# Kernel tuning notes

Hardware: AMD Instinct MI355X
Metric: run time of the kernel (lower is better)

Reference implementation:

```python
import jax, jax.numpy as jnp
import numpy as np

LATENT, H, A, L, BOS = 256, 512, 64, 128, 0


def setup_inputs() -> dict:
    key = jax.random.key(0)
    ks = jax.random.split(key, 20)
    s = 0.05
    return {
        "latent": jax.random.normal(ks[0], (4096, LATENT), jnp.float32),
        "target": jax.random.normal(ks[1], (4096, L, A), jnp.float32),
        # latent dense decoder: Linear(LATENT,H), Tanh, Linear(H,H), Tanh, Linear(H,H)
        "Wd1": jax.random.normal(ks[2], (H, LATENT), jnp.float32) * s,
        "bd1": jnp.zeros((H,), jnp.float32),
        "Wd2": jax.random.normal(ks[3], (H, H), jnp.float32) * s,
        "bd2": jnp.zeros((H,), jnp.float32),
        "Wd3": jax.random.normal(ks[4], (H, H), jnp.float32) * s,
        "bd3": jnp.zeros((H,), jnp.float32),
        # GRU (torch layout: W_ih [3H,A], W_hh [3H,H], gate order r,z,n)
        "W_ih": jax.random.normal(ks[5], (3 * H, A), jnp.float32) * s,
        "W_hh": jax.random.normal(ks[6], (3 * H, H), jnp.float32) * s,
        "b_ih": jnp.zeros((3 * H,), jnp.float32),
        "b_hh": jnp.zeros((3 * H,), jnp.float32),
        # per-step dense decoder: Linear(H,H), Tanh, Linear(H,A), Tanh, Linear(A,A)
        "Wm1": jax.random.normal(ks[7], (H, H), jnp.float32) * s,
        "bm1": jnp.zeros((H,), jnp.float32),
        "Wm2": jax.random.normal(ks[8], (A, H), jnp.float32) * s,
        "bm2": jnp.zeros((A,), jnp.float32),
        "Wm3": jax.random.normal(ks[9], (A, A), jnp.float32) * s,
        "bm3": jnp.zeros((A,), jnp.float32),
    }


def reference(latent, target, Wd1, bd1, Wd2, bd2, Wd3, bd3,
              W_ih, W_hh, b_ih, b_hh, Wm1, bm1, Wm2, bm2, Wm3, bm3):
    B = latent.shape[0]
    # initial hidden from latent: Linear-Tanh-Linear-Tanh-Linear
    h = jnp.tanh(latent @ Wd1.T + bd1)
    h = jnp.tanh(h @ Wd2.T + bd2)
    h = h @ Wd3.T + bd3  # [B, H]

    # BOS pseudo one-hot: -16 everywhere, +16 at BOS index
    bos = jnp.full((B, A), -16.0, jnp.float32).at[:, BOS].set(16.0)

    # teacher forcing: step i (1..L-1) consumes [bos, target[:,1], ..., target[:,L-2]]
    xs = jnp.concatenate([bos[None], jnp.swapaxes(target[:, 1:L - 1], 0, 1)], axis=0)  # [L-1, B, A]

    def step(h, x):
        gi = x @ W_ih.T + b_ih  # [B, 3H]
        gh = h @ W_hh.T + b_hh
        ir, iz, inn = jnp.split(gi, 3, axis=-1)
        hr, hz, hn = jnp.split(gh, 3, axis=-1)
        r = jax.nn.sigmoid(ir + hr)
        z = jax.nn.sigmoid(iz + hz)
        n = jnp.tanh(inn + r * hn)
        h_new = (1.0 - z) * n + z * h
        p = jnp.tanh(h_new @ Wm1.T + bm1)
        p = jnp.tanh(p @ Wm2.T + bm2)
        pred = p @ Wm3.T + bm3  # [B, A]
        return h_new, pred

    _, preds = jax.lax.scan(step, h, xs)  # preds: [L-1, B, A]
    y = jnp.concatenate([bos[None], preds], axis=0)  # [L, B, A]
    return jnp.swapaxes(y, 0, 1)  # [B, L, A]
```

## Files before the change

### kernel.cpp

```cpp
#include <hip/hip_runtime.h>
#include <math.h>
#include <stdint.h>

#define BATCH 4096
#define LATENT 256
#define H 512
#define A 64
#define SEQL 128
#define KCAT 576
#define CT 8

typedef __bf16 bf16x8 __attribute__((ext_vector_type(8)));
typedef float f32x4 __attribute__((ext_vector_type(4)));

__device__ __forceinline__ uint16_t f2bf(float f) {
    union { float f; uint32_t u; } v; v.f = f;
    uint32_t u = v.u + 0x7FFFu + ((v.u >> 16) & 1u);
    return (uint16_t)(u >> 16);
}

__device__ __forceinline__ float fast_sig(float x) {
    return __fdividef(1.0f, 1.0f + __expf(-x));
}
__device__ __forceinline__ float fast_tanh(float x) {
    return __fdividef(2.0f, 1.0f + __expf(-2.0f * x)) - 1.0f;
}

__device__ __forceinline__ f32x4 mfma16(bf16x8 a, bf16x8 b, f32x4 c) {
    return __builtin_amdgcn_mfma_f32_16x16x32_bf16(a, b, c, 0, 0, 0);
}

__device__ __forceinline__ void load_lds16(const void* g, void* l) {
    __builtin_amdgcn_global_load_lds(
        (const __attribute__((address_space(1))) uint32_t*)g,
        (__attribute__((address_space(3))) uint32_t*)l, 16, 0, 0);
}


__global__ __launch_bounds__(256) void cvt_bf16_kernel(const float* __restrict__ src,
                                                       uint16_t* __restrict__ dst, int n) {
    int idx = (blockIdx.x * 256 + threadIdx.x) * 4;
    if (idx < n) {
        float4 v = *(const float4*)(src + idx);
        dst[idx + 0] = f2bf(v.x); dst[idx + 1] = f2bf(v.y);
        dst[idx + 2] = f2bf(v.z); dst[idx + 3] = f2bf(v.w);
    }
}

__global__ __launch_bounds__(256) void wcat_kernel(const float* __restrict__ W_ih,
                                                   const float* __restrict__ W_hh,
                                                   uint16_t* __restrict__ Wcat) {
    int idx = blockIdx.x * 256 + threadIdx.x;
    if (idx < 1536 * KCAT) {
        int row = idx / KCAT, col = idx - row * KCAT;
        float v = (col < 64) ? W_ih[row * 64 + col] : W_hh[row * 512 + col - 64];
        Wcat[idx] = f2bf(v);
    }
}

__global__ __launch_bounds__(256) void bias_kernel(const float* __restrict__ b_ih,
                                                   const float* __restrict__ b_hh,
                                                   float* __restrict__ biases) {
    int idx = blockIdx.x * 256 + threadIdx.x;
    if (idx < 2048) {
        int seg = idx >> 9, j = idx & 511;
        float v;
        if (seg == 0) v = b_ih[j] + b_hh[j];
        else if (seg == 1) v = b_ih[512 + j] + b_hh[512 + j];
        else if (seg == 2) v = b_ih[1024 + j];
        else v = b_hh[1024 + j];
        biases[idx] = v;
    }
}

__global__ __launch_bounds__(256) void bos_kernel(uint16_t* __restrict__ bosb,
                                                  float* __restrict__ out) {
    int idx = blockIdx.x * 256 + threadIdx.x;
    int a = idx & (A - 1);
    int b = idx >> 6;
    float v = (a == 0) ? 16.0f : -16.0f;
    bosb[idx] = f2bf(v);
    out[(size_t)b * SEQL * A + a] = v;
}

template <int BN>
__global__ __launch_bounds__(256)
void gemm_kernel(const uint16_t* __restrict__ Abf, int lda,
                 const uint16_t* __restrict__ Wbf,
                 const float* __restrict__ bias,
                 uint16_t* __restrict__ outb, float* __restrict__ outf,
                 int ldc, int K, int flags, int t0)
{
    __shared__ __align__(16) uint16_t As[128 * 32];
    __shared__ __align__(16) uint16_t Bs[BN * 32];

    const int tid = threadIdx.x;
    const int w = tid >> 6, l = tid & 63;
    const int quad = l >> 4, lan = l & 15;
    const int m0 = blockIdx.y * 128;
    const int n0 = blockIdx.x * BN;

    constexpr int MI = (BN == 128) ? 4 : 2;
    const int wm = (BN == 128) ? ((w >> 1) * 64) : (w * 32);
    const int wn = (BN == 128) ? ((w & 1) * 64) : 0;

    f32x4 acc[MI][4];
#pragma unroll
    for (int i = 0; i < MI; ++i)
#pragma unroll
        for (int j = 0; j < 4; ++j) acc[i][j] = (f32x4){0.f, 0.f, 0.f, 0.f};

    const int arow = (l >> 2);
    const int kc8 = (l & 3) * 8;

    for (int k0 = 0; k0 < K; k0 += 32) {
        __syncthreads();
#pragma unroll
        for (int i = 0; i < 2; ++i) {
            int row = i * 64 + w * 16 + arow;
            load_lds16(Abf + (size_t)(m0 + row) * lda + k0 + kc8,
                       As + i * 2048 + w * 512 + l * 8);
        }
#pragma unroll
        for (int i = 0; i < BN / 64; ++i) {
            int row = i * 64 + w * 16 + arow;
            load_lds16(Wbf + (size_t)(n0 + row) * K + k0 + kc8,
                       Bs + i * 2048 + w * 512 + l * 8);
        }
        __syncthreads();

        bf16x8 af[MI], bf[4];
#pragma unroll
        for (int mi = 0; mi < MI; ++mi)
            af[mi] = *(const bf16x8*)(As + (wm + mi * 16 + lan) * 32 + quad * 8);
#pragma unroll
        for (int nj = 0; nj < 4; ++nj)
            bf[nj] = *(const bf16x8*)(Bs + (wn + nj * 16 + lan) * 32 + quad * 8);
#pragma unroll
        for (int mi = 0; mi < MI; ++mi)
#pragma unroll
            for (int nj = 0; nj < 4; ++nj)
                acc[mi][nj] = mfma16(af[mi], bf[nj], acc[mi][nj]);
    }

    const bool do_tanh = flags & 1;
    const bool mapseq = flags & 2;
#pragma unroll
    for (int mi = 0; mi < MI; ++mi) {
#pragma unroll
        for (int nj = 0; nj < 4; ++nj) {
#pragma unroll
            for (int reg = 0; reg < 4; ++reg) {
                int m = m0 + wm + mi * 16 + quad * 4 + reg;
                int n = n0 + wn + nj * 16 + lan;
                float v = acc[mi][nj][reg] + bias[n];
                if (do_tanh) v = fast_tanh(v);
                if (mapseq) {
                    int b = m & (BATCH - 1), tloc = m >> 12;
                    outf[(size_t)b * SEQL * A + (size_t)(t0 + tloc + 1) * A + n] = v;
                } else {
                    if (outf) outf[(size_t)m * ldc + n] = v;
                    if (outb) outb[(size_t)m * ldc + n] = f2bf(v);
                }
            }
        }
    }
}

__global__ __launch_bounds__(128)
void gru_step_kernel(const uint16_t* __restrict__ xsrc, int sx,
                     const uint16_t* __restrict__ hsrc,
                     const uint16_t* __restrict__ Wcat,
                     const float* __restrict__ biases,
                     const float* __restrict__ hprev,
                     float* __restrict__ hout_f,
                     uint16_t* __restrict__ hout_b)
{
    __shared__ __align__(16) uint16_t As[64 * 32];
    __shared__ __align__(16) uint16_t Bs[192 * 32];

    const int tid = threadIdx.x;
    const int w = tid >> 6, l = tid & 63;
    const int quad = l >> 4, lan = l & 15;
    const int m0 = blockIdx.y * 64;
    const int j0 = blockIdx.x * 64;

    f32x4 acc[2][4][4];
#pragma unroll
    for (int a = 0; a < 2; ++a)
#pragma unroll
        for (int b = 0; b < 4; ++b)
#pragma unroll
            for (int c = 0; c < 4; ++c) acc[a][b][c] = (f32x4){0.f, 0.f, 0.f, 0.f};

    const int arow = (l >> 2);
    const int kc8 = (l & 3) * 8;

    for (int it = 0; it < KCAT / 32; ++it) {
        const int k0 = it * 32;
        const bool xseg = (k0 < 64);
        __syncthreads();
        {
            const uint16_t* src = xseg ? xsrc : hsrc;
            const int stride = xseg ? sx : H;
            const int kc = xseg ? k0 : (k0 - 64);
#pragma unroll
            for (int i = 0; i < 2; ++i) {
                int row = i * 32 + w * 16 + arow;
                load_lds16(src + (size_t)(m0 + row) * stride + kc + kc8,
                           As + i * 1024 + w * 512 + l * 8);
            }
        }
#pragma unroll
        for (int i = 0; i < 6; ++i) {
            int row = i * 32 + w * 16 + arow;
            int g = row >> 6, n = row & 63;
            load_lds16(Wcat + (size_t)((g << 9) + j0 + n) * KCAT + k0 + kc8,
                       Bs + i * 1024 + w * 512 + l * 8);
        }
        __syncthreads();

        bf16x8 af[2];
#pragma unroll
        for (int mi = 0; mi < 2; ++mi)
            af[mi] = *(const bf16x8*)(As + (w * 32 + mi * 16 + lan) * 32 + quad * 8);
#pragma unroll
        for (int g = 0; g < 3; ++g) {
            const int tgt = (g == 2) ? (xseg ? 2 : 3) : g;
#pragma unroll
            for (int nj = 0; nj < 4; ++nj) {
                bf16x8 bfr = *(const bf16x8*)(Bs + (g * 64 + nj * 16 + lan) * 32 + quad * 8);
                acc[0][tgt][nj] = mfma16(af[0], bfr, acc[0][tgt][nj]);
                acc[1][tgt][nj] = mfma16(af[1], bfr, acc[1][tgt][nj]);
            }
        }
    }

    const float* br = biases;
    const float* bz = biases + 512;
    const float* bi = biases + 1024;
    const float* bh = biases + 1536;
#pragma unroll
    for (int mi = 0; mi < 2; ++mi) {
#pragma unroll
        for (int nj = 0; nj < 4; ++nj) {
#pragma unroll
            for (int reg = 0; reg < 4; ++reg) {
                int m = m0 + w * 32 + mi * 16 + quad * 4 + reg;
                int j = j0 + nj * 16 + lan;
                float R = acc[mi][0][nj][reg] + br[j];
                float Z = acc[mi][1][nj][reg] + bz[j];
                float I = acc[mi][2][nj][reg] + bi[j];
                float Hh = acc[mi][3][nj][reg] + bh[j];
                float r = fast_sig(R);
                float z = fast_sig(Z);
                float nn = fast_tanh(I + r * Hh);
                float hp = hprev[(size_t)m * H + j];
                float hv = (1.0f - z) * nn + z * hp;
                hout_f[(size_t)m * H + j] = hv;
                hout_b[(size_t)m * H + j] = f2bf(hv);
            }
        }
    }
}


extern "C" void kernel_launch(void* const* d_in, const int* in_sizes, int n_in,
                              void* d_out, int out_size, void* d_ws, size_t ws_size,
                              hipStream_t stream)
{
    const float* latent = (const float*)d_in[0];
    const float* target = (const float*)d_in[1];
    const float* Wd1 = (const float*)d_in[2];
    const float* bd1 = (const float*)d_in[3];
    const float* Wd2 = (const float*)d_in[4];
    const float* bd2 = (const float*)d_in[5];
    const float* Wd3 = (const float*)d_in[6];
    const float* bd3 = (const float*)d_in[7];
    const float* W_ih = (const float*)d_in[8];
    const float* W_hh = (const float*)d_in[9];
    const float* b_ih = (const float*)d_in[10];
    const float* b_hh = (const float*)d_in[11];
    const float* Wm1 = (const float*)d_in[12];
    const float* bm1 = (const float*)d_in[13];
    const float* Wm2 = (const float*)d_in[14];
    const float* bm2 = (const float*)d_in[15];
    const float* Wm3 = (const float*)d_in[16];
    const float* bm3 = (const float*)d_in[17];

    float* out = (float*)d_out;
    uint8_t* ws = (uint8_t*)d_ws;

    size_t off = 0;
    auto carve = [&](size_t bytes) { void* p = ws + off; off += (bytes + 255) & ~(size_t)255; return p; };
    uint16_t* latb = (uint16_t*)carve((size_t)BATCH * LATENT * 2);
    uint16_t* wd1b = (uint16_t*)carve((size_t)H * LATENT * 2);
    uint16_t* wd2b = (uint16_t*)carve((size_t)H * H * 2);
    uint16_t* wd3b = (uint16_t*)carve((size_t)H * H * 2);
    uint16_t* wm1b = (uint16_t*)carve((size_t)H * H * 2);
    uint16_t* wm2b = (uint16_t*)carve((size_t)A * H * 2);
    uint16_t* wm3b = (uint16_t*)carve((size_t)A * A * 2);
    uint16_t* wcat = (uint16_t*)carve((size_t)1536 * KCAT * 2);
    float* biases  = (float*)carve(2048 * 4);
    uint16_t* bosb = (uint16_t*)carve((size_t)BATCH * A * 2);
    uint16_t* xbf  = (uint16_t*)carve((size_t)BATCH * SEQL * A * 2);
    uint16_t* t1b  = (uint16_t*)carve((size_t)BATCH * H * 2);
    uint16_t* t2b  = (uint16_t*)carve((size_t)BATCH * H * 2);
    uint16_t* h0bf = (uint16_t*)carve((size_t)BATCH * H * 2);
    float* hA      = (float*)carve((size_t)BATCH * H * 4);
    float* hB      = (float*)carve((size_t)BATCH * H * 4);
    uint16_t* hall = (uint16_t*)carve((size_t)CT * BATCH * H * 2);
    uint16_t* p1   = (uint16_t*)carve((size_t)CT * BATCH * H * 2);
    uint16_t* p2   = (uint16_t*)carve((size_t)CT * BATCH * A * 2);
    float* hbuf[2] = {hA, hB};

    dim3 blk256(256), blk128(128);

    auto cvt = [&](const float* s, uint16_t* d, int n) {
        cvt_bf16_kernel<<<dim3((n / 4 + 255) / 256), blk256, 0, stream>>>(s, d, n);
    };
    cvt(latent, latb, BATCH * LATENT);
    cvt(Wd1, wd1b, H * LATENT);
    cvt(Wd2, wd2b, H * H);
    cvt(Wd3, wd3b, H * H);
    cvt(Wm1, wm1b, H * H);
    cvt(Wm2, wm2b, A * H);
    cvt(Wm3, wm3b, A * A);
    cvt(target, xbf, BATCH * SEQL * A);
    wcat_kernel<<<dim3((1536 * KCAT + 255) / 256), blk256, 0, stream>>>(W_ih, W_hh, wcat);
    bias_kernel<<<dim3(8), blk256, 0, stream>>>(b_ih, b_hh, biases);
    bos_kernel<<<dim3(BATCH * A / 256), blk256, 0, stream>>>(bosb, out);

    gemm_kernel<128><<<dim3(H / 128, BATCH / 128), blk256, 0, stream>>>(
        latb, LATENT, wd1b, bd1, t1b, nullptr, H, LATENT, 1, 0);
    gemm_kernel<128><<<dim3(H / 128, BATCH / 128), blk256, 0, stream>>>(
        t1b, H, wd2b, bd2, t2b, nullptr, H, H, 1, 0);
    gemm_kernel<128><<<dim3(H / 128, BATCH / 128), blk256, 0, stream>>>(
        t2b, H, wd3b, bd3, h0bf, hbuf[0], H, H, 0, 0);

    for (int t = 0; t < SEQL - 1; ++t) {
        const uint16_t* xsrc = (t == 0) ? bosb : (xbf + (size_t)t * A);
        const int sx = (t == 0) ? A : (SEQL * A);
        const uint16_t* hsrc = (t == 0) ? h0bf : (hall + (size_t)((t - 1) % CT) * BATCH * H);
        uint16_t* houtb = hall + (size_t)(t % CT) * BATCH * H;

        gru_step_kernel<<<dim3(H / 64, BATCH / 64), blk128, 0, stream>>>(
            xsrc, sx, hsrc, wcat, biases, hbuf[t & 1], hbuf[(t + 1) & 1], houtb);

        if ((t % CT) == CT - 1 || t == SEQL - 2) {
            const int t0c = (t / CT) * CT;
            const int ctc = t - t0c + 1;
            const int M = ctc * BATCH;
            gemm_kernel<128><<<dim3(H / 128, M / 128), blk256, 0, stream>>>(
                hall, H, wm1b, bm1, p1, nullptr, H, H, 1, 0);
            gemm_kernel<64><<<dim3(1, M / 128), blk256, 0, stream>>>(
                p1, H, wm2b, bm2, p2, nullptr, A, H, 1, 0);
            gemm_kernel<64><<<dim3(1, M / 128), blk256, 0, stream>>>(
                p2, A, wm3b, bm3, nullptr, out, A, A, 2, t0c);
        }
    }
}
```

Baseline: 4.193 ms.

## Retile GRU step kernel, pre-layout inputs per step, fuse final two dense layers

The GRU step kernel moves from 64x64 tiles with 128 threads to 128-row by 32-hidden tiles with 256 threads, and the gate weights are loaded as 96 rows per block. The teacher-forcing inputs, BOS row included, are converted once into a contiguous step-major bf16 buffer, so each step reads unit-stride rows. The Wm2 and Wm3 layers are fused into one kernel that keeps the intermediate in LDS, which drops the p2 buffer and one launch per chunk. Together these aim to raise per-step MFMA work per wave and cut global traffic, at the cost of more registers and fewer blocks per step (512 vs 512, same count).

```diff
diff --git a/kernel.cpp b/kernel.cpp
--- a/kernel.cpp
+++ b/kernel.cpp
@@ -9,6 +9,7 @@
 #define SEQL 128
 #define KCAT 576
 #define CT 8
+#define NSTEP 127
 
 typedef __bf16 bf16x8 __attribute__((ext_vector_type(8)));
 typedef float f32x4 __attribute__((ext_vector_type(4)));
@@ -73,40 +74,53 @@
     }
 }
 
-__global__ __launch_bounds__(256) void bos_kernel(uint16_t* __restrict__ bosb,
-                                                  float* __restrict__ out) {
+__global__ __launch_bounds__(256) void xall_kernel(const float* __restrict__ target,
+                                                   uint16_t* __restrict__ X) {
+    int idx = blockIdx.x * 256 + threadIdx.x;
+    int e = idx * 4;
+    int a = e & 63;
+    int b = (e >> 6) & (BATCH - 1);
+    int t = e >> 18;
+    ushort4 o;
+    if (t == 0) {
+        o.x = f2bf((a == 0) ? 16.0f : -16.0f);
+        uint16_t m16 = f2bf(-16.0f);
+        o.y = m16; o.z = m16; o.w = m16;
+    } else {
+        float4 v = *(const float4*)(target + ((size_t)b * SEQL + t) * A + a);
+        o.x = f2bf(v.x); o.y = f2bf(v.y); o.z = f2bf(v.z); o.w = f2bf(v.w);
+    }
+    *(ushort4*)(X + e) = o;
+}
+
+__global__ __launch_bounds__(256) void bosout_kernel(float* __restrict__ out) {
     int idx = blockIdx.x * 256 + threadIdx.x;
     int a = idx & (A - 1);
     int b = idx >> 6;
-    float v = (a == 0) ? 16.0f : -16.0f;
-    bosb[idx] = f2bf(v);
-    out[(size_t)b * SEQL * A + a] = v;
-}
-
-template <int BN>
+    out[(size_t)b * SEQL * A + a] = (a == 0) ? 16.0f : -16.0f;
+}
+
 __global__ __launch_bounds__(256)
 void gemm_kernel(const uint16_t* __restrict__ Abf, int lda,
                  const uint16_t* __restrict__ Wbf,
                  const float* __restrict__ bias,
                  uint16_t* __restrict__ outb, float* __restrict__ outf,
-                 int ldc, int K, int flags, int t0)
+                 int ldc, int K, int do_tanh)
 {
     __shared__ __align__(16) uint16_t As[128 * 32];
-    __shared__ __align__(16) uint16_t Bs[BN * 32];
+    __shared__ __align__(16) uint16_t Bs[128 * 32];
 
     const int tid = threadIdx.x;
     const int w = tid >> 6, l = tid & 63;
     const int quad = l >> 4, lan = l & 15;
     const int m0 = blockIdx.y * 128;
-    const int n0 = blockIdx.x * BN;
-
-    constexpr int MI = (BN == 128) ? 4 : 2;
-    const int wm = (BN == 128) ? ((w >> 1) * 64) : (w * 32);
-    const int wn = (BN == 128) ? ((w & 1) * 64) : 0;
-
-    f32x4 acc[MI][4];
-#pragma unroll
-    for (int i = 0; i < MI; ++i)
+    const int n0 = blockIdx.x * 128;
+    const int wm = (w >> 1) * 64;
+    const int wn = (w & 1) * 64;
+
+    f32x4 acc[4][4];
+#pragma unroll
+    for (int i = 0; i < 4; ++i)
 #pragma unroll
         for (int j = 0; j < 4; ++j) acc[i][j] = (f32x4){0.f, 0.f, 0.f, 0.f};
 
@@ -122,31 +136,29 @@
                        As + i * 2048 + w * 512 + l * 8);
         }
 #pragma unroll
-        for (int i = 0; i < BN / 64; ++i) {
+        for (int i = 0; i < 2; ++i) {
             int row = i * 64 + w * 16 + arow;
             load_lds16(Wbf + (size_t)(n0 + row) * K + k0 + kc8,
                        Bs + i * 2048 + w * 512 + l * 8);
         }
         __syncthreads();
 
-        bf16x8 af[MI], bf[4];
-#pragma unroll
-        for (int mi = 0; mi < MI; ++mi)
+        bf16x8 af[4], bf[4];
+#pragma unroll
+        for (int mi = 0; mi < 4; ++mi)
             af[mi] = *(const bf16x8*)(As + (wm + mi * 16 + lan) * 32 + quad * 8);
 #pragma unroll
         for (int nj = 0; nj < 4; ++nj)
             bf[nj] = *(const bf16x8*)(Bs + (wn + nj * 16 + lan) * 32 + quad * 8);
 #pragma unroll
-        for (int mi = 0; mi < MI; ++mi)
+        for (int mi = 0; mi < 4; ++mi)
 #pragma unroll
             for (int nj = 0; nj < 4; ++nj)
                 acc[mi][nj] = mfma16(af[mi], bf[nj], acc[mi][nj]);
     }
 
-    const bool do_tanh = flags & 1;
-    const bool mapseq = flags & 2;
-#pragma unroll
-    for (int mi = 0; mi < MI; ++mi) {
+#pragma unroll
+    for (int mi = 0; mi < 4; ++mi) {
 #pragma unroll
         for (int nj = 0; nj < 4; ++nj) {
 #pragma unroll
@@ -155,113 +167,221 @@
                 int n = n0 + wn + nj * 16 + lan;
                 float v = acc[mi][nj][reg] + bias[n];
                 if (do_tanh) v = fast_tanh(v);
-                if (mapseq) {
-                    int b = m & (BATCH - 1), tloc = m >> 12;
-                    outf[(size_t)b * SEQL * A + (size_t)(t0 + tloc + 1) * A + n] = v;
-                } else {
-                    if (outf) outf[(size_t)m * ldc + n] = v;
-                    if (outb) outb[(size_t)m * ldc + n] = f2bf(v);
-                }
+                if (outf) outf[(size_t)m * ldc + n] = v;
+                if (outb) outb[(size_t)m * ldc + n] = f2bf(v);
             }
         }
     }
 }
 
-__global__ __launch_bounds__(128)
-void gru_step_kernel(const uint16_t* __restrict__ xsrc, int sx,
-                     const uint16_t* __restrict__ hsrc,
+__global__ __launch_bounds__(256)
+void gru_step_kernel(const uint16_t* __restrict__ xb,
+                     const uint16_t* __restrict__ hbf,
                      const uint16_t* __restrict__ Wcat,
                      const float* __restrict__ biases,
                      const float* __restrict__ hprev,
                      float* __restrict__ hout_f,
                      uint16_t* __restrict__ hout_b)
 {
-    __shared__ __align__(16) uint16_t As[64 * 32];
-    __shared__ __align__(16) uint16_t Bs[192 * 32];
+    __shared__ __align__(16) uint16_t As[128 * 32];
+    __shared__ __align__(16) uint16_t Bs[96 * 32];
 
     const int tid = threadIdx.x;
     const int w = tid >> 6, l = tid & 63;
     const int quad = l >> 4, lan = l & 15;
-    const int m0 = blockIdx.y * 64;
-    const int j0 = blockIdx.x * 64;
-
-    f32x4 acc[2][4][4];
-#pragma unroll
-    for (int a = 0; a < 2; ++a)
-#pragma unroll
-        for (int b = 0; b < 4; ++b)
-#pragma unroll
-            for (int c = 0; c < 4; ++c) acc[a][b][c] = (f32x4){0.f, 0.f, 0.f, 0.f};
-
-    const int arow = (l >> 2);
-    const int kc8 = (l & 3) * 8;
+    const int m0 = blockIdx.y * 128;
+    const int j0 = blockIdx.x * 32;
+    const int wm = (w >> 1) * 64;
+    const int wj = (w & 1) * 16;
+
+    f32x4 acc[4][4];
+#pragma unroll
+    for (int i = 0; i < 4; ++i)
+#pragma unroll
+        for (int j = 0; j < 4; ++j) acc[i][j] = (f32x4){0.f, 0.f, 0.f, 0.f};
 
     for (int it = 0; it < KCAT / 32; ++it) {
         const int k0 = it * 32;
         const bool xseg = (k0 < 64);
         __syncthreads();
+#pragma unroll
+        for (int i = 0; i < 2; ++i) {
+            int g = i * 256 + tid;
+            int row = g >> 2, kc = (g & 3) * 8;
+            const uint16_t* src = xseg
+                ? (xb  + (size_t)(m0 + row) * 64  + k0 + kc)
+                : (hbf + (size_t)(m0 + row) * 512 + (k0 - 64) + kc);
+            load_lds16(src, As + (size_t)g * 8);
+        }
         {
-            const uint16_t* src = xseg ? xsrc : hsrc;
-            const int stride = xseg ? sx : H;
-            const int kc = xseg ? k0 : (k0 - 64);
-#pragma unroll
-            for (int i = 0; i < 2; ++i) {
-                int row = i * 32 + w * 16 + arow;
-                load_lds16(src + (size_t)(m0 + row) * stride + kc + kc8,
-                           As + i * 1024 + w * 512 + l * 8);
+            int g = tid;
+            int row = g >> 2, kc = (g & 3) * 8;
+            int wrow = ((row >> 5) << 9) + j0 + (row & 31);
+            load_lds16(Wcat + (size_t)wrow * KCAT + k0 + kc, Bs + (size_t)g * 8);
+        }
+        if (w < 2) {
+            int g = 256 + tid;
+            int row = g >> 2, kc = (g & 3) * 8;
+            int wrow = ((row >> 5) << 9) + j0 + (row & 31);
+            load_lds16(Wcat + (size_t)wrow * KCAT + k0 + kc, Bs + (size_t)g * 8);
+        }
+        __syncthreads();
+
+        bf16x8 af[4], bfr[3];
+#pragma unroll
+        for (int mi = 0; mi < 4; ++mi)
+            af[mi] = *(const bf16x8*)(As + (wm + mi * 16 + lan) * 32 + quad * 8);
+#pragma unroll
+        for (int g = 0; g < 3; ++g)
+            bfr[g] = *(const bf16x8*)(Bs + (g * 32 + wj + lan) * 32 + quad * 8);
+
+#pragma unroll
+        for (int mi = 0; mi < 4; ++mi) {
+            acc[mi][0] = mfma16(af[mi], bfr[0], acc[mi][0]);
+            acc[mi][1] = mfma16(af[mi], bfr[1], acc[mi][1]);
+        }
+        if (xseg) {
+#pragma unroll
+            for (int mi = 0; mi < 4; ++mi)
+                acc[mi][2] = mfma16(af[mi], bfr[2], acc[mi][2]);
+        } else {
+#pragma unroll
+            for (int mi = 0; mi < 4; ++mi)
+                acc[mi][3] = mfma16(af[mi], bfr[2], acc[mi][3]);
+        }
+    }
+
+    const int j = j0 + wj + lan;
+    const float br = biases[j], bz = biases[512 + j];
+    const float bi = biases[1024 + j], bh = biases[1536 + j];
+#pragma unroll
+    for (int mi = 0; mi < 4; ++mi) {
+#pragma unroll
+        for (int reg = 0; reg < 4; ++reg) {
+            int m = m0 + wm + mi * 16 + quad * 4 + reg;
+            float R  = acc[mi][0][reg] + br;
+            float Z  = acc[mi][1][reg] + bz;
+            float I  = acc[mi][2][reg] + bi;
+            float HN = acc[mi][3][reg] + bh;
+            float r = fast_sig(R);
+            float z = fast_sig(Z);
+            float nn = fast_tanh(I + r * HN);
+            float hp = hprev[(size_t)m * H + j];
+            float hv = (1.0f - z) * nn + z * hp;
+            hout_f[(size_t)m * H + j] = hv;
+            hout_b[(size_t)m * H + j] = f2bf(hv);
+        }
+    }
+}
+
+__global__ __launch_bounds__(256)
+void d23_kernel(const uint16_t* __restrict__ p1,
+                const uint16_t* __restrict__ Wm2,
+                const float* __restrict__ bm2,
+                const uint16_t* __restrict__ Wm3,
+                const float* __restrict__ bm3,
+                float* __restrict__ out, int t0)
+{
+    __shared__ __align__(16) uint16_t As[128 * 32];
+    __shared__ __align__(16) uint16_t B2[64 * 32];
+    __shared__ __align__(16) uint16_t W3[64 * 64];
+    __shared__ __align__(16) uint16_t Ps[128 * 80];
+
+    const int tid = threadIdx.x;
+    const int w = tid >> 6, l = tid & 63;
+    const int quad = l >> 4, lan = l & 15;
+    const int m0 = blockIdx.y * 128;
+    const int wm = w * 32;
+
+#pragma unroll
+    for (int i = 0; i < 2; ++i) {
+        int g = i * 256 + tid;
+        int row = g >> 3, kc = (g & 7) * 8;
+        load_lds16(Wm3 + (size_t)row * 64 + kc, W3 + (size_t)g * 8);
+    }
+
+    f32x4 acc[2][4];
+#pragma unroll
+    for (int i = 0; i < 2; ++i)
+#pragma unroll
+        for (int j = 0; j < 4; ++j) acc[i][j] = (f32x4){0.f, 0.f, 0.f, 0.f};
+
+    for (int k0 = 0; k0 < 512; k0 += 32) {
+        __syncthreads();
+#pragma unroll
+        for (int i = 0; i < 2; ++i) {
+            int g = i * 256 + tid;
+            int row = g >> 2, kc = (g & 3) * 8;
+            load_lds16(p1 + (size_t)(m0 + row) * 512 + k0 + kc, As + (size_t)g * 8);
+        }
+        {
+            int g = tid;
+            int row = g >> 2, kc = (g & 3) * 8;
+            load_lds16(Wm2 + (size_t)row * 512 + k0 + kc, B2 + (size_t)g * 8);
+        }
+        __syncthreads();
+
+        bf16x8 af[2], bf[4];
+#pragma unroll
+        for (int mi = 0; mi < 2; ++mi)
+            af[mi] = *(const bf16x8*)(As + (wm + mi * 16 + lan) * 32 + quad * 8);
+#pragma unroll
+        for (int nj = 0; nj < 4; ++nj)
+            bf[nj] = *(const bf16x8*)(B2 + (nj * 16 + lan) * 32 + quad * 8);
+#pragma unroll
+        for (int mi = 0; mi < 2; ++mi)
+#pragma unroll
+            for (int nj = 0; nj < 4; ++nj)
+                acc[mi][nj] = mfma16(af[mi], bf[nj], acc[mi][nj]);
+    }
+
+#pragma unroll
+    for (int mi = 0; mi < 2; ++mi)
+#pragma unroll
+        for (int nj = 0; nj < 4; ++nj)
+#pragma unroll
+            for (int reg = 0; reg < 4; ++reg) {
+                int row = wm + mi * 16 + quad * 4 + reg;
+                int n = nj * 16 + lan;
+                float v = fast_tanh(acc[mi][nj][reg] + bm2[n]);
+                Ps[row * 80 + n] = f2bf(v);
             }
-        }
-#pragma unroll
-        for (int i = 0; i < 6; ++i) {
-            int row = i * 32 + w * 16 + arow;
-            int g = row >> 6, n = row & 63;
-            load_lds16(Wcat + (size_t)((g << 9) + j0 + n) * KCAT + k0 + kc8,
-                       Bs + i * 1024 + w * 512 + l * 8);
-        }
-        __syncthreads();
-
-        bf16x8 af[2];
+    __syncthreads();
+
+    f32x4 a3[2][4];
+#pragma unroll
+    for (int i = 0; i < 2; ++i)
+#pragma unroll
+        for (int j = 0; j < 4; ++j) a3[i][j] = (f32x4){0.f, 0.f, 0.f, 0.f};
+
+#pragma unroll
+    for (int ks = 0; ks < 64; ks += 32) {
+        bf16x8 af[2], bf[4];
 #pragma unroll
         for (int mi = 0; mi < 2; ++mi)
-            af[mi] = *(const bf16x8*)(As + (w * 32 + mi * 16 + lan) * 32 + quad * 8);
-#pragma unroll
-        for (int g = 0; g < 3; ++g) {
-            const int tgt = (g == 2) ? (xseg ? 2 : 3) : g;
-#pragma unroll
-            for (int nj = 0; nj < 4; ++nj) {
-                bf16x8 bfr = *(const bf16x8*)(Bs + (g * 64 + nj * 16 + lan) * 32 + quad * 8);
-                acc[0][tgt][nj] = mfma16(af[0], bfr, acc[0][tgt][nj]);
-                acc[1][tgt][nj] = mfma16(af[1], bfr, acc[1][tgt][nj]);
+            af[mi] = *(const bf16x8*)(Ps + (wm + mi * 16 + lan) * 80 + ks + quad * 8);
+#pragma unroll
+        for (int nj = 0; nj < 4; ++nj)
+            bf[nj] = *(const bf16x8*)(W3 + (nj * 16 + lan) * 64 + ks + quad * 8);
+#pragma unroll
+        for (int mi = 0; mi < 2; ++mi)
+#pragma unroll
+            for (int nj = 0; nj < 4; ++nj)
+                a3[mi][nj] = mfma16(af[mi], bf[nj], a3[mi][nj]);
+    }
+
+#pragma unroll
+    for (int mi = 0; mi < 2; ++mi)
+#pragma unroll
+        for (int nj = 0; nj < 4; ++nj)
+#pragma unroll
+            for (int reg = 0; reg < 4; ++reg) {
+                int m = m0 + wm + mi * 16 + quad * 4 + reg;
+                int n = nj * 16 + lan;
+                int b = m & (BATCH - 1), tl = m >> 12;
+                out[(size_t)b * SEQL * A + (size_t)(t0 + tl + 1) * A + n] =
+                    a3[mi][nj][reg] + bm3[n];
             }
-        }
-    }
-
-    const float* br = biases;
-    const float* bz = biases + 512;
-    const float* bi = biases + 1024;
-    const float* bh = biases + 1536;
-#pragma unroll
-    for (int mi = 0; mi < 2; ++mi) {
-#pragma unroll
-        for (int nj = 0; nj < 4; ++nj) {
-#pragma unroll
-            for (int reg = 0; reg < 4; ++reg) {
-                int m = m0 + w * 32 + mi * 16 + quad * 4 + reg;
-                int j = j0 + nj * 16 + lan;
-                float R = acc[mi][0][nj][reg] + br[j];
-                float Z = acc[mi][1][nj][reg] + bz[j];
-                float I = acc[mi][2][nj][reg] + bi[j];
-                float Hh = acc[mi][3][nj][reg] + bh[j];
-                float r = fast_sig(R);
-                float z = fast_sig(Z);
-                float nn = fast_tanh(I + r * Hh);
-                float hp = hprev[(size_t)m * H + j];
-                float hv = (1.0f - z) * nn + z * hp;
-                hout_f[(size_t)m * H + j] = hv;
-                hout_b[(size_t)m * H + j] = f2bf(hv);
-            }
-        }
-    }
 }
 
 
@@ -302,8 +422,7 @@
     uint16_t* wm3b = (uint16_t*)carve((size_t)A * A * 2);
     uint16_t* wcat = (uint16_t*)carve((size_t)1536 * KCAT * 2);
     float* biases  = (float*)carve(2048 * 4);
-    uint16_t* bosb = (uint16_t*)carve((size_t)BATCH * A * 2);
-    uint16_t* xbf  = (uint16_t*)carve((size_t)BATCH * SEQL * A * 2);
+    uint16_t* Xall = (uint16_t*)carve((size_t)NSTEP * BATCH * A * 2);
     uint16_t* t1b  = (uint16_t*)carve((size_t)BATCH * H * 2);
     uint16_t* t2b  = (uint16_t*)carve((size_t)BATCH * H * 2);
     uint16_t* h0bf = (uint16_t*)carve((size_t)BATCH * H * 2);
@@ -311,13 +430,12 @@
     float* hB      = (float*)carve((size_t)BATCH * H * 4);
     uint16_t* hall = (uint16_t*)carve((size_t)CT * BATCH * H * 2);
     uint16_t* p1   = (uint16_t*)carve((size_t)CT * BATCH * H * 2);
-    uint16_t* p2   = (uint16_t*)carve((size_t)CT * BATCH * A * 2);
     float* hbuf[2] = {hA, hB};
 
-    dim3 blk256(256), blk128(128);
+    dim3 blk(256);
 
     auto cvt = [&](const float* s, uint16_t* d, int n) {
-        cvt_bf16_kernel<<<dim3((n / 4 + 255) / 256), blk256, 0, stream>>>(s, d, n);
+        cvt_bf16_kernel<<<dim3((n / 4 + 255) / 256), blk, 0, stream>>>(s, d, n);
     };
     cvt(latent, latb, BATCH * LATENT);
     cvt(Wd1, wd1b, H * LATENT);
@@ -326,37 +444,31 @@
     cvt(Wm1, wm1b, H * H);
     cvt(Wm2, wm2b, A * H);
     cvt(Wm3, wm3b, A * A);
-    cvt(target, xbf, BATCH * SEQL * A);
-    wcat_kernel<<<dim3((1536 * KCAT + 255) / 256), blk256, 0, stream>>>(W_ih, W_hh, wcat);
-    bias_kernel<<<dim3(8), blk256, 0, stream>>>(b_ih, b_hh, biases);
-    bos_kernel<<<dim3(BATCH * A / 256), blk256, 0, stream>>>(bosb, out);
-
-    gemm_kernel<128><<<dim3(H / 128, BATCH / 128), blk256, 0, stream>>>(
-        latb, LATENT, wd1b, bd1, t1b, nullptr, H, LATENT, 1, 0);
-    gemm_kernel<128><<<dim3(H / 128, BATCH / 128), blk256, 0, stream>>>(
-        t1b, H, wd2b, bd2, t2b, nullptr, H, H, 1, 0);
-    gemm_kernel<128><<<dim3(H / 128, BATCH / 128), blk256, 0, stream>>>(
-        t2b, H, wd3b, bd3, h0bf, hbuf[0], H, H, 0, 0);
-
-    for (int t = 0; t < SEQL - 1; ++t) {
-        const uint16_t* xsrc = (t == 0) ? bosb : (xbf + (size_t)t * A);
-        const int sx = (t == 0) ? A : (SEQL * A);
-        const uint16_t* hsrc = (t == 0) ? h0bf : (hall + (size_t)((t - 1) % CT) * BATCH * H);
-        uint16_t* houtb = hall + (size_t)(t % CT) * BATCH * H;
-
-        gru_step_kernel<<<dim3(H / 64, BATCH / 64), blk128, 0, stream>>>(
-            xsrc, sx, hsrc, wcat, biases, hbuf[t & 1], hbuf[(t + 1) & 1], houtb);
-
-        if ((t % CT) == CT - 1 || t == SEQL - 2) {
-            const int t0c = (t / CT) * CT;
-            const int ctc = t - t0c + 1;
-            const int M = ctc * BATCH;
-            gemm_kernel<128><<<dim3(H / 128, M / 128), blk256, 0, stream>>>(
-                hall, H, wm1b, bm1, p1, nullptr, H, H, 1, 0);
-            gemm_kernel<64><<<dim3(1, M / 128), blk256, 0, stream>>>(
-                p1, H, wm2b, bm2, p2, nullptr, A, H, 1, 0);
-            gemm_kernel<64><<<dim3(1, M / 128), blk256, 0, stream>>>(
-                p2, A, wm3b, bm3, nullptr, out, A, A, 2, t0c);
-        }
-    }
-}
+    wcat_kernel<<<dim3((1536 * KCAT + 255) / 256), blk, 0, stream>>>(W_ih, W_hh, wcat);
+    bias_kernel<<<dim3(8), blk, 0, stream>>>(b_ih, b_hh, biases);
+    xall_kernel<<<dim3(NSTEP * BATCH * A / 4 / 256), blk, 0, stream>>>(target, Xall);
+    bosout_kernel<<<dim3(BATCH * A / 256), blk, 0, stream>>>(out);
+
+    gemm_kernel<<<dim3(H / 128, BATCH / 128), blk, 0, stream>>>(
+        latb, LATENT, wd1b, bd1, t1b, nullptr, H, LATENT, 1);
+    gemm_kernel<<<dim3(H / 128, BATCH / 128), blk, 0, stream>>>(
+        t1b, H, wd2b, bd2, t2b, nullptr, H, H, 1);
+    gemm_kernel<<<dim3(H / 128, BATCH / 128), blk, 0, stream>>>(
+        t2b, H, wd3b, bd3, h0bf, hA, H, H, 0);
+
+    for (int c = 0; c < 16; ++c) {
+        const int ct = (c == 15) ? 7 : 8;
+        const int M = ct * BATCH;
+        for (int tl = 0; tl < ct; ++tl) {
+            const int t = c * CT + tl;
+            const uint16_t* hbf = (t == 0) ? h0bf : (hall + (size_t)((t - 1) & 7) * BATCH * H);
+            gru_step_kernel<<<dim3(16, 32), blk, 0, stream>>>(
+                Xall + (size_t)t * BATCH * A, hbf, wcat, biases,
+                hbuf[t & 1], hbuf[(t + 1) & 1], hall + (size_t)tl * BATCH * H);
+        }
+        gemm_kernel<<<dim3(H / 128, M / 128), blk, 0, stream>>>(
+            hall, H, wm1b, bm1, p1, nullptr, H, H, 1);
+        d23_kernel<<<dim3(1, M / 128), blk, 0, stream>>>(
+            p1, wm2b, bm2, wm3b, bm3, out, c * CT);
+    }
+}
```

Measured after the change: 3.555 ms. 1.18x faster.
